# Kernel optimization log

Measured on AMD Instinct MI355X. Metric: run time of the kernel, lower is better.

Reference implementation:

```python
import jax, jax.numpy as jnp
import numpy as np

B, N, K, H = 2, 2048, 48, 128
SCALE = 30.0
LN_EPS = 1e-5


def _gather_nodes(nodes, idx):
    # nodes: [B,N,H], idx: [B,N,K] -> [B,N,K,H]
    return nodes[jnp.arange(nodes.shape[0])[:, None, None], idx]


def _ln(x, g, b):
    m = jnp.mean(x, axis=-1, keepdims=True)
    v = jnp.mean(jnp.square(x - m), axis=-1, keepdims=True)
    return (x - m) * jax.lax.rsqrt(v + LN_EPS) * g + b


def _gelu(x):
    return jax.nn.gelu(x, approximate=False)  # torch.nn.GELU default (erf)


def setup_inputs() -> dict:
    key = jax.random.key(0)
    ks = jax.random.split(key, 24)
    d = {}
    d["h_V"] = jax.random.normal(ks[0], (B, N, H), jnp.float32)
    d["h_E"] = jax.random.normal(ks[1], (B, N, K, H), jnp.float32)
    d["E_idx"] = jax.random.randint(ks[2], (B, N, K), 0, N)
    d["mask_V"] = (jax.random.uniform(ks[3], (B, N)) > 0.1).astype(jnp.float32)
    d["mask_attend"] = (jax.random.uniform(ks[4], (B, N, K)) > 0.1).astype(jnp.float32)
    s = 0.05
    # message MLP (node update): W1 in = 3H
    d["W1_w"] = s * jax.random.normal(ks[5], (3 * H, H), jnp.float32)
    d["W1_b"] = jnp.zeros((H,), jnp.float32)
    d["W2_w"] = s * jax.random.normal(ks[6], (H, H), jnp.float32)
    d["W2_b"] = jnp.zeros((H,), jnp.float32)
    d["W3_w"] = s * jax.random.normal(ks[7], (H, H), jnp.float32)
    d["W3_b"] = jnp.zeros((H,), jnp.float32)
    # message MLP (edge update)
    d["W11_w"] = s * jax.random.normal(ks[8], (3 * H, H), jnp.float32)
    d["W11_b"] = jnp.zeros((H,), jnp.float32)
    d["W12_w"] = s * jax.random.normal(ks[9], (H, H), jnp.float32)
    d["W12_b"] = jnp.zeros((H,), jnp.float32)
    d["W13_w"] = s * jax.random.normal(ks[10], (H, H), jnp.float32)
    d["W13_b"] = jnp.zeros((H,), jnp.float32)
    # FFN
    d["Win_w"] = s * jax.random.normal(ks[11], (H, 4 * H), jnp.float32)
    d["Win_b"] = jnp.zeros((4 * H,), jnp.float32)
    d["Wout_w"] = s * jax.random.normal(ks[12], (4 * H, H), jnp.float32)
    d["Wout_b"] = jnp.zeros((H,), jnp.float32)
    # layernorms
    for i, nm in enumerate(["ln1", "ln2", "ln3"]):
        d[nm + "_g"] = jnp.ones((H,), jnp.float32)
        d[nm + "_b"] = jnp.zeros((H,), jnp.float32)
    return d


def reference(h_V, h_E, E_idx, mask_V, mask_attend,
              W1_w, W1_b, W2_w, W2_b, W3_w, W3_b,
              W11_w, W11_b, W12_w, W12_b, W13_w, W13_b,
              Win_w, Win_b, Wout_w, Wout_b,
              ln1_g, ln1_b, ln2_g, ln2_b, ln3_g, ln3_b):
    # --- node message pass ---
    h_EV = jnp.concatenate([
        jnp.broadcast_to(h_V[:, :, None, :], h_E.shape),
        h_E,
        _gather_nodes(h_V, E_idx),
    ], axis=-1)  # [B,N,K,3H]
    h_msg = _gelu(h_EV @ W1_w + W1_b)
    h_msg = _gelu(h_msg @ W2_w + W2_b)
    h_msg = h_msg @ W3_w + W3_b
    h_msg = mask_attend[..., None] * h_msg
    dh = jnp.sum(h_msg, axis=-2) / SCALE  # [B,N,H]
    h_Vn = _ln(h_V + dh, ln1_g, ln1_b)
    # --- FFN ---
    dh = _gelu(h_Vn @ Win_w + Win_b) @ Wout_w + Wout_b
    h_Vn = _ln(h_Vn + dh, ln2_g, ln2_b)
    h_Vn = mask_V[..., None] * h_Vn
    # --- edge update ---
    h_EV2 = jnp.concatenate([
        jnp.broadcast_to(h_Vn[:, :, None, :], h_E.shape),
        h_E,
        _gather_nodes(h_Vn, E_idx),
    ], axis=-1)
    h_msg2 = _gelu(h_EV2 @ W11_w + W11_b)
    h_msg2 = _gelu(h_msg2 @ W12_w + W12_b)
    h_msg2 = h_msg2 @ W13_w + W13_b
    h_En = _ln(h_E + h_msg2, ln3_g, ln3_b)
    return (h_Vn, h_En)
```

## Files before the change

kernel.cpp:

```cpp
#include <hip/hip_runtime.h>
#include <hip/hip_bf16.h>

#define DEVINL __device__ __forceinline__

typedef __attribute__((ext_vector_type(8))) short short8;
typedef __attribute__((ext_vector_type(4))) float f32x4;

DEVINL unsigned short f2bf(float x) {
  __hip_bfloat16 h = __float2bfloat16(x);
  return __builtin_bit_cast(unsigned short, h);
}
DEVINL unsigned int pk2(float lo, float hi) {
  return (unsigned int)f2bf(lo) | ((unsigned int)f2bf(hi) << 16);
}
DEVINL float bf2f(unsigned short h) {
  union { unsigned int u; float f; } c; c.u = ((unsigned int)h) << 16;
  return c.f;
}
DEVINL float gelu_f(float x) {
  const float u = x * x;
  const float y = x * (0.7978845608f + 0.0356774081f * u);
  const float e = __expf(-2.0f * y);
  return x * __builtin_amdgcn_rcpf(1.0f + e);
}
DEVINL f32x4 mfma16(short8 a, short8 b, f32x4 c) {
  return __builtin_amdgcn_mfma_f32_16x16x32_bf16(a, b, c, 0, 0, 0);
}

template<int KSTEPS, int MT, int NT>
DEVINL void gemm_tiles(const unsigned short* Xl, int ldx,
                       const unsigned short* __restrict__ Wp,
                       int lane, int w, f32x4 (&acc)[MT][2])
{
  const int rr = lane & 15;
  const int kg = (lane >> 4) << 3;
  __builtin_amdgcn_s_setprio(1);
  #pragma unroll
  for (int t = 0; t < KSTEPS; ++t) {
    short8 a[MT];
    #pragma unroll
    for (int m = 0; m < MT; ++m)
      a[m] = *(const short8*)(Xl + (m * 16 + rr) * ldx + t * 32 + kg);
    #pragma unroll
    for (int c = 0; c < 2; ++c) {
      short8 bf = *(const short8*)(Wp + ((size_t)(t * NT + (w * 2 + c)) * 64 + lane) * 8);
      #pragma unroll
      for (int m = 0; m < MT; ++m)
        acc[m][c] = mfma16(a[m], bf, acc[m][c]);
    }
  }
  __builtin_amdgcn_s_setprio(0);
}

__global__ __launch_bounds__(256) void k_pack(
    const float* __restrict__ W1w,  const float* __restrict__ W2w,
    const float* __restrict__ W3w,  const float* __restrict__ W11w,
    const float* __restrict__ W12w, const float* __restrict__ W13w,
    const float* __restrict__ Winw, const float* __restrict__ Woutw,
    unsigned short* __restrict__ dst)
{
  const int f = blockIdx.x * 256 + threadIdx.x;
  if (f >= 36864) return;
  const float* src; int row0 = 0, Ncols = 128, NT = 8, lf;
  if (f < 20480) {
    const int seg = f >> 11; lf = f & 2047;
    switch (seg) {
      case 0: src = W1w;  row0 = 0;   break;
      case 1: src = W1w;  row0 = 128; break;
      case 2: src = W1w;  row0 = 256; break;
      case 3: src = W2w;  break;
      case 4: src = W3w;  break;
      case 5: src = W11w; row0 = 0;   break;
      case 6: src = W11w; row0 = 128; break;
      case 7: src = W11w; row0 = 256; break;
      case 8: src = W12w; break;
      default: src = W13w; break;
    }
  } else if (f < 28672) { src = Winw; lf = f - 20480; NT = 32; Ncols = 512; }
  else { src = Woutw; lf = f - 28672; }
  const int l = lf & 63;
  const int g = lf >> 6;
  const int c = g % NT;
  const int t = g / NT;
  const int r0 = row0 + t * 32 + ((l >> 4) << 3);
  const int col = c * 16 + (l & 15);
  short8 vv;
  #pragma unroll
  for (int b = 0; b < 8; ++b)
    vv[b] = (short)f2bf(src[(size_t)(r0 + b) * Ncols + col]);
  *(short8*)(dst + (size_t)f * 8) = vv;
}

__global__ __launch_bounds__(256) void k_pre(
    const float* __restrict__ X,
    const unsigned short* __restrict__ Wtp,
    const unsigned short* __restrict__ Wbp,
    const float* __restrict__ bias,
    float* __restrict__ P1, unsigned short* __restrict__ P3)
{
  __shared__ __align__(16) unsigned short Xs2[16 * 136];
  const int tid = threadIdx.x;
  const int lane = tid & 63;
  const int w = tid >> 6;
  const int rr = lane & 15;
  const int kg = (lane >> 4) << 3;
  const int row0 = blockIdx.x * 16;

  for (int e = tid; e < 512; e += 256) {
    const int r = e >> 5, q = (e & 31) << 2;
    float4 v = *(const float4*)(X + (size_t)(row0 + r) * 128 + q);
    uint2 pk; pk.x = pk2(v.x, v.y); pk.y = pk2(v.z, v.w);
    *(uint2*)(&Xs2[r * 136 + q]) = pk;
  }
  __syncthreads();

  const f32x4 zf = {0.f, 0.f, 0.f, 0.f};
  f32x4 a0[2] = {zf, zf}, a1[2] = {zf, zf};
  #pragma unroll
  for (int t = 0; t < 4; ++t) {
    const short8 a = *(const short8*)(&Xs2[rr * 136 + t * 32 + kg]);
    #pragma unroll
    for (int c = 0; c < 2; ++c) {
      short8 bt = *(const short8*)(Wtp + ((size_t)(t * 8 + (w * 2 + c)) * 64 + lane) * 8);
      a0[c] = mfma16(a, bt, a0[c]);
      short8 bb = *(const short8*)(Wbp + ((size_t)(t * 8 + (w * 2 + c)) * 64 + lane) * 8);
      a1[c] = mfma16(a, bb, a1[c]);
    }
  }
  #pragma unroll
  for (int c = 0; c < 2; ++c) {
    const int col = w * 32 + c * 16 + rr;
    const float b = bias[col];
    #pragma unroll
    for (int r = 0; r < 4; ++r) {
      const int row = row0 + ((lane >> 4) << 2) + r;
      P1[(size_t)row * 128 + col] = a0[c][r] + b;
      P3[(size_t)row * 128 + col] = f2bf(a1[c][r]);
    }
  }
}

template<bool HEB>
__global__ __launch_bounds__(256) void k_node_t(
    const float* __restrict__ hV, const float* __restrict__ hE,
    unsigned short* __restrict__ hEbOut,
    const int* __restrict__ Eidx, const float* __restrict__ maskA,
    const float* __restrict__ P1g, const unsigned short* __restrict__ P3g,
    const unsigned short* __restrict__ Wmidp,
    const unsigned short* __restrict__ W2p, const float* __restrict__ W2b,
    const unsigned short* __restrict__ W3p, const float* __restrict__ W3b,
    const float* __restrict__ ln1g, const float* __restrict__ ln1b,
    float* __restrict__ hVn1)
{
  __shared__ __align__(16) unsigned short Xs[48 * 136];
  __shared__ __align__(16) unsigned short Ms[48 * 136];
  __shared__ float maskv[48];
  __shared__ float dhs[128];
  __shared__ float red[2];

  const int tid = threadIdx.x;
  const int lane = tid & 63;
  const int w = tid >> 6;
  const int rr = lane & 15;
  const int g4 = (lane >> 4) << 2;
  const int bidx = (blockIdx.x & 7) * 512 + (blockIdx.x >> 3);
  const int bbase = bidx & ~2047;

  const float* hErow = hE + (size_t)bidx * 6144;
  const int* idxr = Eidx + (size_t)bidx * 48;

  if (tid < 48) maskv[tid] = maskA[(size_t)bidx * 48 + tid];

  for (int e = tid; e < 1536; e += 256) {
    const int r = e >> 5, q = (e & 31) << 2;
    float4 v = *(const float4*)(hErow + r * 128 + q);
    uint2 pk; pk.x = pk2(v.x, v.y); pk.y = pk2(v.z, v.w);
    *(uint2*)(&Xs[r * 136 + q]) = pk;
    if constexpr (HEB)
      *(uint2*)(hEbOut + (size_t)bidx * 6144 + r * 128 + q) = pk;
  }
  for (int e = tid; e < 768; e += 256) {
    const int r = e >> 4, q = (e & 15) << 3;
    const int j = idxr[r];
    *(short8*)(&Ms[r * 136 + q]) = *(const short8*)(P3g + (size_t)(bbase + j) * 128 + q);
  }
  const float p1c0 = P1g[(size_t)bidx * 128 + w * 32 + rr];
  const float p1c1 = P1g[(size_t)bidx * 128 + w * 32 + 16 + rr];
  __syncthreads();

  f32x4 acc[3][2];
  #pragma unroll
  for (int m = 0; m < 3; ++m)
    #pragma unroll
    for (int c = 0; c < 2; ++c)
      #pragma unroll
      for (int r = 0; r < 4; ++r) {
        const int row = m * 16 + g4 + r;
        const int col = w * 32 + c * 16 + rr;
        acc[m][c][r] = (c ? p1c1 : p1c0) + bf2f(Ms[row * 136 + col]);
      }

  gemm_tiles<4, 3, 8>(Xs, 136, Wmidp, lane, w, acc);
  #pragma unroll
  for (int m = 0; m < 3; ++m)
    #pragma unroll
    for (int c = 0; c < 2; ++c)
      #pragma unroll
      for (int r = 0; r < 4; ++r) {
        const int row = m * 16 + g4 + r;
        Ms[row * 136 + w * 32 + c * 16 + rr] = f2bf(gelu_f(acc[m][c][r]));
      }
  __syncthreads();

  const f32x4 zf = {0.f, 0.f, 0.f, 0.f};
  #pragma unroll
  for (int m = 0; m < 3; ++m) { acc[m][0] = zf; acc[m][1] = zf; }
  gemm_tiles<4, 3, 8>(Ms, 136, W2p, lane, w, acc);
  {
    const float b0 = W2b[w * 32 + rr], b1 = W2b[w * 32 + 16 + rr];
    #pragma unroll
    for (int m = 0; m < 3; ++m)
      #pragma unroll
      for (int c = 0; c < 2; ++c)
        #pragma unroll
        for (int r = 0; r < 4; ++r) {
          const int row = m * 16 + g4 + r;
          Xs[row * 136 + w * 32 + c * 16 + rr] = f2bf(gelu_f(acc[m][c][r] + (c ? b1 : b0)));
        }
  }
  __syncthreads();

  #pragma unroll
  for (int m = 0; m < 3; ++m) { acc[m][0] = zf; acc[m][1] = zf; }
  gemm_tiles<4, 3, 8>(Xs, 136, W3p, lane, w, acc);

  {
    const float b0 = W3b[w * 32 + rr], b1 = W3b[w * 32 + 16 + rr];
    float p0 = 0.f, p1 = 0.f;
    #pragma unroll
    for (int m = 0; m < 3; ++m)
      #pragma unroll
      for (int r = 0; r < 4; ++r) {
        const float mk = maskv[m * 16 + g4 + r];
        p0 += mk * (acc[m][0][r] + b0);
        p1 += mk * (acc[m][1][r] + b1);
      }
    p0 += __shfl_xor(p0, 16); p0 += __shfl_xor(p0, 32);
    p1 += __shfl_xor(p1, 16); p1 += __shfl_xor(p1, 32);
    if (lane < 16) { dhs[w * 32 + lane] = p0; dhs[w * 32 + 16 + lane] = p1; }
  }
  __syncthreads();

  if (tid < 64) {
    const float x0 = hV[(size_t)bidx * 128 + tid]      + dhs[tid]      * (1.0f / 30.0f);
    const float x1 = hV[(size_t)bidx * 128 + 64 + tid] + dhs[tid + 64] * (1.0f / 30.0f);
    float s = x0 + x1, q2 = x0 * x0 + x1 * x1;
    #pragma unroll
    for (int msk = 1; msk < 64; msk <<= 1) {
      s += __shfl_xor(s, msk);
      q2 += __shfl_xor(q2, msk);
    }
    if (tid == 0) {
      const float mean = s * (1.f / 128.f);
      red[0] = mean;
      red[1] = rsqrtf(q2 * (1.f / 128.f) - mean * mean + 1e-5f);
    }
  }
  __syncthreads();
  if (tid < 128) {
    const float x = hV[(size_t)bidx * 128 + tid] + dhs[tid] * (1.0f / 30.0f);
    hVn1[(size_t)bidx * 128 + tid] = (x - red[0]) * red[1] * ln1g[tid] + ln1b[tid];
  }
}

__global__ __launch_bounds__(256) void k_ffn(
    const float* __restrict__ hVn1,
    const unsigned short* __restrict__ Winp, const float* __restrict__ Winb,
    const unsigned short* __restrict__ Woutp, const float* __restrict__ Woutb,
    const float* __restrict__ ln2g, const float* __restrict__ ln2b,
    const float* __restrict__ maskV,
    const unsigned short* __restrict__ W11tp, const unsigned short* __restrict__ W11bp,
    const float* __restrict__ W11b,
    float* __restrict__ outV, float* __restrict__ P1, unsigned short* __restrict__ P3)
{
  __shared__ __align__(16) unsigned short Xs2[16 * 136];
  __shared__ __align__(16) unsigned short Ys[16 * 520];
  __shared__ __align__(16) unsigned short Ts[16 * 136];
  __shared__ float Rs[16 * 128];

  const int tid = threadIdx.x;
  const int lane = tid & 63;
  const int w = tid >> 6;
  const int rr = lane & 15;
  const int kg = (lane >> 4) << 3;
  const int row0 = blockIdx.x * 16;

  for (int e = tid; e < 512; e += 256) {
    const int r = e >> 5, q = (e & 31) << 2;
    float4 v = *(const float4*)(hVn1 + (size_t)(row0 + r) * 128 + q);
    uint2 pk; pk.x = pk2(v.x, v.y); pk.y = pk2(v.z, v.w);
    *(uint2*)(&Xs2[r * 136 + q]) = pk;
  }
  __syncthreads();

  const f32x4 zf = {0.f, 0.f, 0.f, 0.f};
  f32x4 acc1[8];
  #pragma unroll
  for (int c = 0; c < 8; ++c) acc1[c] = zf;
  #pragma unroll
  for (int t = 0; t < 4; ++t) {
    const short8 a = *(const short8*)(&Xs2[rr * 136 + t * 32 + kg]);
    #pragma unroll
    for (int c = 0; c < 8; ++c) {
      const short8 bf = *(const short8*)(Winp + ((size_t)(t * 32 + w * 8 + c) * 64 + lane) * 8);
      acc1[c] = mfma16(a, bf, acc1[c]);
    }
  }
  #pragma unroll
  for (int c = 0; c < 8; ++c) {
    const int col = w * 128 + c * 16 + rr;
    const float bias = Winb[col];
    #pragma unroll
    for (int r = 0; r < 4; ++r) {
      const int row = ((lane >> 4) << 2) + r;
      Ys[row * 520 + col] = f2bf(gelu_f(acc1[c][r] + bias));
    }
  }
  __syncthreads();

  f32x4 acc2[2];
  acc2[0] = zf; acc2[1] = zf;
  #pragma unroll 4
  for (int t = 0; t < 16; ++t) {
    const short8 a = *(const short8*)(&Ys[rr * 520 + t * 32 + kg]);
    #pragma unroll
    for (int c = 0; c < 2; ++c) {
      const short8 bf = *(const short8*)(Woutp + ((size_t)(t * 8 + w * 2 + c) * 64 + lane) * 8);
      acc2[c] = mfma16(a, bf, acc2[c]);
    }
  }
  #pragma unroll
  for (int c = 0; c < 2; ++c) {
    const int col = w * 32 + c * 16 + rr;
    const float bias = Woutb[col];
    #pragma unroll
    for (int r = 0; r < 4; ++r) {
      const int row = ((lane >> 4) << 2) + r;
      Rs[row * 128 + col] = acc2[c][r] + bias + hVn1[(size_t)(row0 + row) * 128 + col];
    }
  }
  __syncthreads();

  const float g0 = ln2g[lane], g1 = ln2g[lane + 64];
  const float be0 = ln2b[lane], be1 = ln2b[lane + 64];
  for (int i = 0; i < 4; ++i) {
    const int row = w * 4 + i;
    const int grow = row0 + row;
    const float x0 = Rs[row * 128 + lane], x1 = Rs[row * 128 + 64 + lane];
    float s = x0 + x1, q2 = x0 * x0 + x1 * x1;
    #pragma unroll
    for (int msk = 1; msk < 64; msk <<= 1) {
      s += __shfl_xor(s, msk);
      q2 += __shfl_xor(q2, msk);
    }
    const float mean = s * (1.f / 128.f);
    const float rstd = rsqrtf(q2 * (1.f / 128.f) - mean * mean + 1e-5f);
    const float mv = maskV[grow];
    const float y0 = ((x0 - mean) * rstd * g0 + be0) * mv;
    const float y1 = ((x1 - mean) * rstd * g1 + be1) * mv;
    outV[(size_t)grow * 128 + lane]      = y0;
    outV[(size_t)grow * 128 + 64 + lane] = y1;
    Ts[row * 136 + lane]      = f2bf(y0);
    Ts[row * 136 + 64 + lane] = f2bf(y1);
  }
  __syncthreads();

  f32x4 a0[2] = {zf, zf}, a1[2] = {zf, zf};
  #pragma unroll
  for (int t = 0; t < 4; ++t) {
    const short8 a = *(const short8*)(&Ts[rr * 136 + t * 32 + kg]);
    #pragma unroll
    for (int c = 0; c < 2; ++c) {
      short8 bt = *(const short8*)(W11tp + ((size_t)(t * 8 + (w * 2 + c)) * 64 + lane) * 8);
      a0[c] = mfma16(a, bt, a0[c]);
      short8 bb = *(const short8*)(W11bp + ((size_t)(t * 8 + (w * 2 + c)) * 64 + lane) * 8);
      a1[c] = mfma16(a, bb, a1[c]);
    }
  }
  #pragma unroll
  for (int c = 0; c < 2; ++c) {
    const int col = w * 32 + c * 16 + rr;
    const float b = W11b[col];
    #pragma unroll
    for (int r = 0; r < 4; ++r) {
      const int row = row0 + ((lane >> 4) << 2) + r;
      P1[(size_t)row * 128 + col] = a0[c][r] + b;
      P3[(size_t)row * 128 + col] = f2bf(a1[c][r]);
    }
  }
}

template<bool HEB>
__global__ __launch_bounds__(256) void k_edge_t(
    const float* __restrict__ hE, const unsigned short* __restrict__ hEb,
    const int* __restrict__ Eidx,
    const float* __restrict__ P1g, const unsigned short* __restrict__ P3g,
    const unsigned short* __restrict__ Wmidp,
    const unsigned short* __restrict__ W12p, const float* __restrict__ W12b,
    const unsigned short* __restrict__ W13p, const float* __restrict__ W13b,
    const float* __restrict__ ln3g, const float* __restrict__ ln3b,
    float* __restrict__ outE)
{
  __shared__ __align__(16) unsigned short Xs[48 * 136];
  __shared__ __align__(16) unsigned short Ms[48 * 136];
  __shared__ float sums[48 * 4];
  __shared__ float sqs[48 * 4];
  __shared__ float mr[96];

  const int tid = threadIdx.x;
  const int lane = tid & 63;
  const int w = tid >> 6;
  const int rr = lane & 15;
  const int g4 = (lane >> 4) << 2;
  const int bidx = (blockIdx.x & 7) * 512 + (blockIdx.x >> 3);
  const int bbase = bidx & ~2047;

  const int* idxr = Eidx + (size_t)bidx * 48;

  if constexpr (HEB) {
    for (int e = tid; e < 768; e += 256) {
      const int r = e >> 4, q = (e & 15) << 3;
      *(short8*)(&Xs[r * 136 + q]) = *(const short8*)(hEb + (size_t)bidx * 6144 + r * 128 + q);
    }
  } else {
    const float* hErow = hE + (size_t)bidx * 6144;
    for (int e = tid; e < 1536; e += 256) {
      const int r = e >> 5, q = (e & 31) << 2;
      float4 v = *(const float4*)(hErow + r * 128 + q);
      uint2 pk; pk.x = pk2(v.x, v.y); pk.y = pk2(v.z, v.w);
      *(uint2*)(&Xs[r * 136 + q]) = pk;
    }
  }
  for (int e = tid; e < 768; e += 256) {
    const int r = e >> 4, q = (e & 15) << 3;
    const int j = idxr[r];
    *(short8*)(&Ms[r * 136 + q]) = *(const short8*)(P3g + (size_t)(bbase + j) * 128 + q);
  }
  const float p1c0 = P1g[(size_t)bidx * 128 + w * 32 + rr];
  const float p1c1 = P1g[(size_t)bidx * 128 + w * 32 + 16 + rr];
  __syncthreads();

  f32x4 acc[3][2];
  float res[3][2][4];
  #pragma unroll
  for (int m = 0; m < 3; ++m)
    #pragma unroll
    for (int c = 0; c < 2; ++c)
      #pragma unroll
      for (int r = 0; r < 4; ++r) {
        const int row = m * 16 + g4 + r;
        const int col = w * 32 + c * 16 + rr;
        acc[m][c][r] = (c ? p1c1 : p1c0) + bf2f(Ms[row * 136 + col]);
        res[m][c][r] = bf2f(Xs[row * 136 + col]);
      }

  gemm_tiles<4, 3, 8>(Xs, 136, Wmidp, lane, w, acc);
  #pragma unroll
  for (int m = 0; m < 3; ++m)
    #pragma unroll
    for (int c = 0; c < 2; ++c)
      #pragma unroll
      for (int r = 0; r < 4; ++r) {
        const int row = m * 16 + g4 + r;
        Ms[row * 136 + w * 32 + c * 16 + rr] = f2bf(gelu_f(acc[m][c][r]));
      }
  __syncthreads();

  const f32x4 zf = {0.f, 0.f, 0.f, 0.f};
  #pragma unroll
  for (int m = 0; m < 3; ++m) { acc[m][0] = zf; acc[m][1] = zf; }
  gemm_tiles<4, 3, 8>(Ms, 136, W12p, lane, w, acc);
  {
    const float b0 = W12b[w * 32 + rr], b1 = W12b[w * 32 + 16 + rr];
    #pragma unroll
    for (int m = 0; m < 3; ++m)
      #pragma unroll
      for (int c = 0; c < 2; ++c)
        #pragma unroll
        for (int r = 0; r < 4; ++r) {
          const int row = m * 16 + g4 + r;
          Xs[row * 136 + w * 32 + c * 16 + rr] = f2bf(gelu_f(acc[m][c][r] + (c ? b1 : b0)));
        }
  }
  __syncthreads();

  #pragma unroll
  for (int m = 0; m < 3; ++m) { acc[m][0] = zf; acc[m][1] = zf; }
  gemm_tiles<4, 3, 8>(Xs, 136, W13p, lane, w, acc);

  {
    const float b0 = W13b[w * 32 + rr], b1 = W13b[w * 32 + 16 + rr];
    #pragma unroll
    for (int m = 0; m < 3; ++m)
      #pragma unroll
      for (int r = 0; r < 4; ++r) {
        const int row = m * 16 + g4 + r;
        acc[m][0][r] += b0 + res[m][0][r];
        acc[m][1][r] += b1 + res[m][1][r];
        float s = acc[m][0][r] + acc[m][1][r];
        float q2 = acc[m][0][r] * acc[m][0][r] + acc[m][1][r] * acc[m][1][r];
        s += __shfl_xor(s, 1); q2 += __shfl_xor(q2, 1);
        s += __shfl_xor(s, 2); q2 += __shfl_xor(q2, 2);
        s += __shfl_xor(s, 4); q2 += __shfl_xor(q2, 4);
        s += __shfl_xor(s, 8); q2 += __shfl_xor(q2, 8);
        if ((lane & 15) == 0) { sums[row * 4 + w] = s; sqs[row * 4 + w] = q2; }
      }
  }
  __syncthreads();
  if (tid < 48) {
    const float s = sums[tid * 4] + sums[tid * 4 + 1] + sums[tid * 4 + 2] + sums[tid * 4 + 3];
    const float q2 = sqs[tid * 4] + sqs[tid * 4 + 1] + sqs[tid * 4 + 2] + sqs[tid * 4 + 3];
    const float mean = s * (1.f / 128.f);
    mr[tid * 2] = mean;
    mr[tid * 2 + 1] = rsqrtf(q2 * (1.f / 128.f) - mean * mean + 1e-5f);
  }
  __syncthreads();
  {
    const float g0 = ln3g[w * 32 + rr], g1 = ln3g[w * 32 + 16 + rr];
    const float be0 = ln3b[w * 32 + rr], be1 = ln3b[w * 32 + 16 + rr];
    #pragma unroll
    for (int m = 0; m < 3; ++m)
      #pragma unroll
      for (int r = 0; r < 4; ++r) {
        const int row = m * 16 + g4 + r;
        const float mean = mr[row * 2], rstd = mr[row * 2 + 1];
        const size_t base = (size_t)bidx * 6144 + (size_t)row * 128 + w * 32 + rr;
        outE[base]      = (acc[m][0][r] - mean) * rstd * g0 + be0;
        outE[base + 16] = (acc[m][1][r] - mean) * rstd * g1 + be1;
      }
  }
}

extern "C" void kernel_launch(void* const* d_in, const int* in_sizes, int n_in,
                              void* d_out, int out_size, void* d_ws, size_t ws_size,
                              hipStream_t stream) {
  const float* hV    = (const float*)d_in[0];
  const float* hE    = (const float*)d_in[1];
  const int*   Eidx  = (const int*)d_in[2];
  const float* maskV = (const float*)d_in[3];
  const float* maskA = (const float*)d_in[4];
  const float* W1w  = (const float*)d_in[5];  const float* W1b  = (const float*)d_in[6];
  const float* W2w  = (const float*)d_in[7];  const float* W2b  = (const float*)d_in[8];
  const float* W3w  = (const float*)d_in[9];  const float* W3b  = (const float*)d_in[10];
  const float* W11w = (const float*)d_in[11]; const float* W11b = (const float*)d_in[12];
  const float* W12w = (const float*)d_in[13]; const float* W12b = (const float*)d_in[14];
  const float* W13w = (const float*)d_in[15]; const float* W13b = (const float*)d_in[16];
  const float* Winw = (const float*)d_in[17]; const float* Winb = (const float*)d_in[18];
  const float* Woutw= (const float*)d_in[19]; const float* Woutb= (const float*)d_in[20];
  const float* ln1g = (const float*)d_in[21]; const float* ln1b = (const float*)d_in[22];
  const float* ln2g = (const float*)d_in[23]; const float* ln2b = (const float*)d_in[24];
  const float* ln3g = (const float*)d_in[25]; const float* ln3b = (const float*)d_in[26];

  float* outV = (float*)d_out;
  float* outE = outV + (size_t)4096 * 128;

  char* ws = (char*)d_ws;
  float* hVn1 = (float*)ws;
  float* P1   = (float*)(ws + (size_t)2 * 1024 * 1024);
  unsigned short* P3 = (unsigned short*)(ws + (size_t)4 * 1024 * 1024);
  unsigned short* Wp = (unsigned short*)(ws + (size_t)5 * 1024 * 1024);
  unsigned short* hEb = (unsigned short*)(ws + (size_t)6 * 1024 * 1024);

  const size_t NEED = (size_t)6 * 1024 * 1024 + (size_t)4096 * 48 * 128 * 2;
  const bool heb = ws_size >= NEED;

  const unsigned short* W1top_p  = Wp;
  const unsigned short* W1mid_p  = Wp + (size_t)2048 * 8;
  const unsigned short* W1bot_p  = Wp + (size_t)4096 * 8;
  const unsigned short* W2p      = Wp + (size_t)6144 * 8;
  const unsigned short* W3p      = Wp + (size_t)8192 * 8;
  const unsigned short* W11top_p = Wp + (size_t)10240 * 8;
  const unsigned short* W11mid_p = Wp + (size_t)12288 * 8;
  const unsigned short* W11bot_p = Wp + (size_t)14336 * 8;
  const unsigned short* W12p     = Wp + (size_t)16384 * 8;
  const unsigned short* W13p     = Wp + (size_t)18432 * 8;
  const unsigned short* Winp     = Wp + (size_t)20480 * 8;
  const unsigned short* Woutp    = Wp + (size_t)28672 * 8;

  k_pack<<<144, 256, 0, stream>>>(W1w, W2w, W3w, W11w, W12w, W13w, Winw, Woutw, Wp);
  k_pre<<<256, 256, 0, stream>>>(hV, W1top_p, W1bot_p, W1b, P1, P3);

  if (heb)
    k_node_t<true><<<4096, 256, 0, stream>>>(hV, hE, hEb, Eidx, maskA, P1, P3,
                                             W1mid_p, W2p, W2b, W3p, W3b,
                                             ln1g, ln1b, hVn1);
  else
    k_node_t<false><<<4096, 256, 0, stream>>>(hV, hE, hEb, Eidx, maskA, P1, P3,
                                              W1mid_p, W2p, W2b, W3p, W3b,
                                              ln1g, ln1b, hVn1);

  k_ffn<<<256, 256, 0, stream>>>(hVn1, Winp, Winb, Woutp, Woutb,
                                 ln2g, ln2b, maskV,
                                 W11top_p, W11bot_p, W11b,
                                 outV, P1, P3);

  if (heb)
    k_edge_t<true><<<4096, 256, 0, stream>>>(hE, hEb, Eidx, P1, P3,
                                             W11mid_p, W12p, W12b, W13p, W13b,
                                             ln3g, ln3b, outE);
  else
    k_edge_t<false><<<4096, 256, 0, stream>>>(hE, hEb, Eidx, P1, P3,
                                              W11mid_p, W12p, W12b, W13p, W13b,
                                              ln3g, ln3b, outE);
}
```

Measured before the change: 142.9 us.

## Stream h_E directly into MFMA fragments and drop the Xs LDS buffer

```diff
diff --git a/kernel.cpp b/kernel.cpp
--- a/kernel.cpp
+++ b/kernel.cpp
@@ -140,10 +140,10 @@
   }
 }
 
-template<bool HEB>
-__global__ __launch_bounds__(256) void k_node_t(
+template<bool HEBW>
+__global__ __launch_bounds__(256, 6) void k_node_t(
     const float* __restrict__ hV, const float* __restrict__ hE,
-    unsigned short* __restrict__ hEbOut,
+    unsigned short* __restrict__ hEb,
     const int* __restrict__ Eidx, const float* __restrict__ maskA,
     const float* __restrict__ P1g, const unsigned short* __restrict__ P3g,
     const unsigned short* __restrict__ Wmidp,
@@ -152,43 +152,62 @@
     const float* __restrict__ ln1g, const float* __restrict__ ln1b,
     float* __restrict__ hVn1)
 {
-  __shared__ __align__(16) unsigned short Xs[48 * 136];
   __shared__ __align__(16) unsigned short Ms[48 * 136];
   __shared__ float maskv[48];
   __shared__ float dhs[128];
-  __shared__ float red[2];
 
   const int tid = threadIdx.x;
   const int lane = tid & 63;
   const int w = tid >> 6;
   const int rr = lane & 15;
   const int g4 = (lane >> 4) << 2;
+  const int kg = (lane >> 4) << 3;
   const int bidx = (blockIdx.x & 7) * 512 + (blockIdx.x >> 3);
   const int bbase = bidx & ~2047;
-
-  const float* hErow = hE + (size_t)bidx * 6144;
   const int* idxr = Eidx + (size_t)bidx * 48;
 
   if (tid < 48) maskv[tid] = maskA[(size_t)bidx * 48 + tid];
-
-  for (int e = tid; e < 1536; e += 256) {
-    const int r = e >> 5, q = (e & 31) << 2;
-    float4 v = *(const float4*)(hErow + r * 128 + q);
-    uint2 pk; pk.x = pk2(v.x, v.y); pk.y = pk2(v.z, v.w);
-    *(uint2*)(&Xs[r * 136 + q]) = pk;
-    if constexpr (HEB)
-      *(uint2*)(hEbOut + (size_t)bidx * 6144 + r * 128 + q) = pk;
-  }
-  for (int e = tid; e < 768; e += 256) {
+  #pragma unroll
+  for (int i = 0; i < 3; ++i) {
+    const int e = i * 256 + tid;
     const int r = e >> 4, q = (e & 15) << 3;
     const int j = idxr[r];
     *(short8*)(&Ms[r * 136 + q]) = *(const short8*)(P3g + (size_t)(bbase + j) * 128 + q);
   }
   const float p1c0 = P1g[(size_t)bidx * 128 + w * 32 + rr];
   const float p1c1 = P1g[(size_t)bidx * 128 + w * 32 + 16 + rr];
-  __syncthreads();
-
+
+  const f32x4 zf = {0.f, 0.f, 0.f, 0.f};
   f32x4 acc[3][2];
+  #pragma unroll
+  for (int m = 0; m < 3; ++m) { acc[m][0] = zf; acc[m][1] = zf; }
+  {
+    const float* Arow = hE + (size_t)bidx * 6144;
+    unsigned short* Hrow = hEb + (size_t)bidx * 6144;
+    __builtin_amdgcn_s_setprio(1);
+    #pragma unroll
+    for (int t = 0; t < 4; ++t) {
+      const short8 bf0 = *(const short8*)(Wmidp + ((size_t)(t * 8 + w * 2) * 64 + lane) * 8);
+      const short8 bf1 = *(const short8*)(Wmidp + ((size_t)(t * 8 + w * 2 + 1) * 64 + lane) * 8);
+      #pragma unroll
+      for (int m = 0; m < 3; ++m) {
+        const float* p = Arow + (m * 16 + rr) * 128 + t * 32 + kg;
+        float4 v0 = *(const float4*)p;
+        float4 v1 = *(const float4*)(p + 4);
+        uint4 pk;
+        pk.x = pk2(v0.x, v0.y); pk.y = pk2(v0.z, v0.w);
+        pk.z = pk2(v1.x, v1.y); pk.w = pk2(v1.z, v1.w);
+        if (HEBW && w == 0)
+          *(uint4*)(Hrow + (m * 16 + rr) * 128 + t * 32 + kg) = pk;
+        const short8 a = __builtin_bit_cast(short8, pk);
+        acc[m][0] = mfma16(a, bf0, acc[m][0]);
+        acc[m][1] = mfma16(a, bf1, acc[m][1]);
+      }
+    }
+    __builtin_amdgcn_s_setprio(0);
+  }
+  __syncthreads();
+
   #pragma unroll
   for (int m = 0; m < 3; ++m)
     #pragma unroll
@@ -197,10 +216,21 @@
       for (int r = 0; r < 4; ++r) {
         const int row = m * 16 + g4 + r;
         const int col = w * 32 + c * 16 + rr;
-        acc[m][c][r] = (c ? p1c1 : p1c0) + bf2f(Ms[row * 136 + col]);
-      }
-
-  gemm_tiles<4, 3, 8>(Xs, 136, Wmidp, lane, w, acc);
+        const float v = acc[m][c][r] + (c ? p1c1 : p1c0) + bf2f(Ms[row * 136 + col]);
+        Ms[row * 136 + col] = f2bf(gelu_f(v));
+      }
+  __syncthreads();
+
+  {
+    const float b0 = W2b[w * 32 + rr], b1 = W2b[w * 32 + 16 + rr];
+    #pragma unroll
+    for (int m = 0; m < 3; ++m) {
+      acc[m][0] = (f32x4){b0, b0, b0, b0};
+      acc[m][1] = (f32x4){b1, b1, b1, b1};
+    }
+  }
+  gemm_tiles<4, 3, 8>(Ms, 136, W2p, lane, w, acc);
+  __syncthreads();
   #pragma unroll
   for (int m = 0; m < 3; ++m)
     #pragma unroll
@@ -212,38 +242,25 @@
       }
   __syncthreads();
 
-  const f32x4 zf = {0.f, 0.f, 0.f, 0.f};
-  #pragma unroll
-  for (int m = 0; m < 3; ++m) { acc[m][0] = zf; acc[m][1] = zf; }
-  gemm_tiles<4, 3, 8>(Ms, 136, W2p, lane, w, acc);
-  {
-    const float b0 = W2b[w * 32 + rr], b1 = W2b[w * 32 + 16 + rr];
-    #pragma unroll
-    for (int m = 0; m < 3; ++m)
-      #pragma unroll
-      for (int c = 0; c < 2; ++c)
-        #pragma unroll
-        for (int r = 0; r < 4; ++r) {
-          const int row = m * 16 + g4 + r;
-          Xs[row * 136 + w * 32 + c * 16 + rr] = f2bf(gelu_f(acc[m][c][r] + (c ? b1 : b0)));
-        }
-  }
-  __syncthreads();
-
-  #pragma unroll
-  for (int m = 0; m < 3; ++m) { acc[m][0] = zf; acc[m][1] = zf; }
-  gemm_tiles<4, 3, 8>(Xs, 136, W3p, lane, w, acc);
-
   {
     const float b0 = W3b[w * 32 + rr], b1 = W3b[w * 32 + 16 + rr];
+    #pragma unroll
+    for (int m = 0; m < 3; ++m) {
+      acc[m][0] = (f32x4){b0, b0, b0, b0};
+      acc[m][1] = (f32x4){b1, b1, b1, b1};
+    }
+  }
+  gemm_tiles<4, 3, 8>(Ms, 136, W3p, lane, w, acc);
+
+  {
     float p0 = 0.f, p1 = 0.f;
     #pragma unroll
     for (int m = 0; m < 3; ++m)
       #pragma unroll
       for (int r = 0; r < 4; ++r) {
         const float mk = maskv[m * 16 + g4 + r];
-        p0 += mk * (acc[m][0][r] + b0);
-        p1 += mk * (acc[m][1][r] + b1);
+        p0 += mk * acc[m][0][r];
+        p1 += mk * acc[m][1][r];
       }
     p0 += __shfl_xor(p0, 16); p0 += __shfl_xor(p0, 32);
     p1 += __shfl_xor(p1, 16); p1 += __shfl_xor(p1, 32);
@@ -251,25 +268,22 @@
   }
   __syncthreads();
 
-  if (tid < 64) {
-    const float x0 = hV[(size_t)bidx * 128 + tid]      + dhs[tid]      * (1.0f / 30.0f);
-    const float x1 = hV[(size_t)bidx * 128 + 64 + tid] + dhs[tid + 64] * (1.0f / 30.0f);
-    float s = x0 + x1, q2 = x0 * x0 + x1 * x1;
+  {
+    const float x0 = hV[(size_t)bidx * 128 + lane]      + dhs[lane]      * (1.0f / 30.0f);
+    const float x1 = hV[(size_t)bidx * 128 + 64 + lane] + dhs[lane + 64] * (1.0f / 30.0f);
+    float s = x0 + x1, sq = x0 * x0 + x1 * x1;
     #pragma unroll
     for (int msk = 1; msk < 64; msk <<= 1) {
       s += __shfl_xor(s, msk);
-      q2 += __shfl_xor(q2, msk);
-    }
-    if (tid == 0) {
-      const float mean = s * (1.f / 128.f);
-      red[0] = mean;
-      red[1] = rsqrtf(q2 * (1.f / 128.f) - mean * mean + 1e-5f);
-    }
-  }
-  __syncthreads();
-  if (tid < 128) {
-    const float x = hV[(size_t)bidx * 128 + tid] + dhs[tid] * (1.0f / 30.0f);
-    hVn1[(size_t)bidx * 128 + tid] = (x - red[0]) * red[1] * ln1g[tid] + ln1b[tid];
+      sq += __shfl_xor(sq, msk);
+    }
+    const float mean = s * (1.f / 128.f);
+    const float rstd = rsqrtf(sq * (1.f / 128.f) - mean * mean + 1e-5f);
+    if (lane < 32) {
+      const int col = w * 32 + lane;
+      const float xx = hV[(size_t)bidx * 128 + col] + dhs[col] * (1.0f / 30.0f);
+      hVn1[(size_t)bidx * 128 + col] = (xx - mean) * rstd * ln1g[col] + ln1b[col];
+    }
   }
 }
 
@@ -401,7 +415,7 @@
 }
 
 template<bool HEB>
-__global__ __launch_bounds__(256) void k_edge_t(
+__global__ __launch_bounds__(256, 6) void k_edge_t(
     const float* __restrict__ hE, const unsigned short* __restrict__ hEb,
     const int* __restrict__ Eidx,
     const float* __restrict__ P1g, const unsigned short* __restrict__ P3g,
@@ -411,7 +425,6 @@
     const float* __restrict__ ln3g, const float* __restrict__ ln3b,
     float* __restrict__ outE)
 {
-  __shared__ __align__(16) unsigned short Xs[48 * 136];
   __shared__ __align__(16) unsigned short Ms[48 * 136];
   __shared__ float sums[48 * 4];
   __shared__ float sqs[48 * 4];
@@ -422,36 +435,53 @@
   const int w = tid >> 6;
   const int rr = lane & 15;
   const int g4 = (lane >> 4) << 2;
+  const int kg = (lane >> 4) << 3;
   const int bidx = (blockIdx.x & 7) * 512 + (blockIdx.x >> 3);
   const int bbase = bidx & ~2047;
-
   const int* idxr = Eidx + (size_t)bidx * 48;
 
-  if constexpr (HEB) {
-    for (int e = tid; e < 768; e += 256) {
-      const int r = e >> 4, q = (e & 15) << 3;
-      *(short8*)(&Xs[r * 136 + q]) = *(const short8*)(hEb + (size_t)bidx * 6144 + r * 128 + q);
-    }
-  } else {
-    const float* hErow = hE + (size_t)bidx * 6144;
-    for (int e = tid; e < 1536; e += 256) {
-      const int r = e >> 5, q = (e & 31) << 2;
-      float4 v = *(const float4*)(hErow + r * 128 + q);
-      uint2 pk; pk.x = pk2(v.x, v.y); pk.y = pk2(v.z, v.w);
-      *(uint2*)(&Xs[r * 136 + q]) = pk;
-    }
-  }
-  for (int e = tid; e < 768; e += 256) {
+  #pragma unroll
+  for (int i = 0; i < 3; ++i) {
+    const int e = i * 256 + tid;
     const int r = e >> 4, q = (e & 15) << 3;
     const int j = idxr[r];
     *(short8*)(&Ms[r * 136 + q]) = *(const short8*)(P3g + (size_t)(bbase + j) * 128 + q);
   }
   const float p1c0 = P1g[(size_t)bidx * 128 + w * 32 + rr];
   const float p1c1 = P1g[(size_t)bidx * 128 + w * 32 + 16 + rr];
-  __syncthreads();
-
+
+  const f32x4 zf = {0.f, 0.f, 0.f, 0.f};
   f32x4 acc[3][2];
-  float res[3][2][4];
+  #pragma unroll
+  for (int m = 0; m < 3; ++m) { acc[m][0] = zf; acc[m][1] = zf; }
+  {
+    __builtin_amdgcn_s_setprio(1);
+    #pragma unroll
+    for (int t = 0; t < 4; ++t) {
+      const short8 bf0 = *(const short8*)(Wmidp + ((size_t)(t * 8 + w * 2) * 64 + lane) * 8);
+      const short8 bf1 = *(const short8*)(Wmidp + ((size_t)(t * 8 + w * 2 + 1) * 64 + lane) * 8);
+      #pragma unroll
+      for (int m = 0; m < 3; ++m) {
+        short8 a;
+        if constexpr (HEB) {
+          a = *(const short8*)(hEb + (size_t)bidx * 6144 + (m * 16 + rr) * 128 + t * 32 + kg);
+        } else {
+          const float* p = hE + (size_t)bidx * 6144 + (m * 16 + rr) * 128 + t * 32 + kg;
+          float4 v0 = *(const float4*)p;
+          float4 v1 = *(const float4*)(p + 4);
+          uint4 pk;
+          pk.x = pk2(v0.x, v0.y); pk.y = pk2(v0.z, v0.w);
+          pk.z = pk2(v1.x, v1.y); pk.w = pk2(v1.z, v1.w);
+          a = __builtin_bit_cast(short8, pk);
+        }
+        acc[m][0] = mfma16(a, bf0, acc[m][0]);
+        acc[m][1] = mfma16(a, bf1, acc[m][1]);
+      }
+    }
+    __builtin_amdgcn_s_setprio(0);
+  }
+  __syncthreads();
+
   #pragma unroll
   for (int m = 0; m < 3; ++m)
     #pragma unroll
@@ -460,11 +490,21 @@
       for (int r = 0; r < 4; ++r) {
         const int row = m * 16 + g4 + r;
         const int col = w * 32 + c * 16 + rr;
-        acc[m][c][r] = (c ? p1c1 : p1c0) + bf2f(Ms[row * 136 + col]);
-        res[m][c][r] = bf2f(Xs[row * 136 + col]);
-      }
-
-  gemm_tiles<4, 3, 8>(Xs, 136, Wmidp, lane, w, acc);
+        const float v = acc[m][c][r] + (c ? p1c1 : p1c0) + bf2f(Ms[row * 136 + col]);
+        Ms[row * 136 + col] = f2bf(gelu_f(v));
+      }
+  __syncthreads();
+
+  {
+    const float b0 = W12b[w * 32 + rr], b1 = W12b[w * 32 + 16 + rr];
+    #pragma unroll
+    for (int m = 0; m < 3; ++m) {
+      acc[m][0] = (f32x4){b0, b0, b0, b0};
+      acc[m][1] = (f32x4){b1, b1, b1, b1};
+    }
+  }
+  gemm_tiles<4, 3, 8>(Ms, 136, W12p, lane, w, acc);
+  __syncthreads();
   #pragma unroll
   for (int m = 0; m < 3; ++m)
     #pragma unroll
@@ -476,46 +516,39 @@
       }
   __syncthreads();
 
-  const f32x4 zf = {0.f, 0.f, 0.f, 0.f};
-  #pragma unroll
-  for (int m = 0; m < 3; ++m) { acc[m][0] = zf; acc[m][1] = zf; }
-  gemm_tiles<4, 3, 8>(Ms, 136, W12p, lane, w, acc);
-  {
-    const float b0 = W12b[w * 32 + rr], b1 = W12b[w * 32 + 16 + rr];
-    #pragma unroll
-    for (int m = 0; m < 3; ++m)
-      #pragma unroll
-      for (int c = 0; c < 2; ++c)
-        #pragma unroll
-        for (int r = 0; r < 4; ++r) {
-          const int row = m * 16 + g4 + r;
-          Xs[row * 136 + w * 32 + c * 16 + rr] = f2bf(gelu_f(acc[m][c][r] + (c ? b1 : b0)));
-        }
-  }
-  __syncthreads();
-
-  #pragma unroll
-  for (int m = 0; m < 3; ++m) { acc[m][0] = zf; acc[m][1] = zf; }
-  gemm_tiles<4, 3, 8>(Xs, 136, W13p, lane, w, acc);
-
   {
     const float b0 = W13b[w * 32 + rr], b1 = W13b[w * 32 + 16 + rr];
     #pragma unroll
-    for (int m = 0; m < 3; ++m)
-      #pragma unroll
-      for (int r = 0; r < 4; ++r) {
-        const int row = m * 16 + g4 + r;
-        acc[m][0][r] += b0 + res[m][0][r];
-        acc[m][1][r] += b1 + res[m][1][r];
-        float s = acc[m][0][r] + acc[m][1][r];
-        float q2 = acc[m][0][r] * acc[m][0][r] + acc[m][1][r] * acc[m][1][r];
-        s += __shfl_xor(s, 1); q2 += __shfl_xor(q2, 1);
-        s += __shfl_xor(s, 2); q2 += __shfl_xor(q2, 2);
-        s += __shfl_xor(s, 4); q2 += __shfl_xor(q2, 4);
-        s += __shfl_xor(s, 8); q2 += __shfl_xor(q2, 8);
-        if ((lane & 15) == 0) { sums[row * 4 + w] = s; sqs[row * 4 + w] = q2; }
-      }
-  }
+    for (int m = 0; m < 3; ++m) {
+      acc[m][0] = (f32x4){b0, b0, b0, b0};
+      acc[m][1] = (f32x4){b1, b1, b1, b1};
+    }
+  }
+  gemm_tiles<4, 3, 8>(Ms, 136, W13p, lane, w, acc);
+
+  #pragma unroll
+  for (int m = 0; m < 3; ++m)
+    #pragma unroll
+    for (int r = 0; r < 4; ++r) {
+      const int row = m * 16 + g4 + r;
+      float r0, r1;
+      if constexpr (HEB) {
+        r0 = bf2f(hEb[(size_t)bidx * 6144 + row * 128 + w * 32 + rr]);
+        r1 = bf2f(hEb[(size_t)bidx * 6144 + row * 128 + w * 32 + 16 + rr]);
+      } else {
+        r0 = hE[(size_t)bidx * 6144 + row * 128 + w * 32 + rr];
+        r1 = hE[(size_t)bidx * 6144 + row * 128 + w * 32 + 16 + rr];
+      }
+      acc[m][0][r] += r0;
+      acc[m][1][r] += r1;
+      float s = acc[m][0][r] + acc[m][1][r];
+      float q2 = acc[m][0][r] * acc[m][0][r] + acc[m][1][r] * acc[m][1][r];
+      s += __shfl_xor(s, 1); q2 += __shfl_xor(q2, 1);
+      s += __shfl_xor(s, 2); q2 += __shfl_xor(q2, 2);
+      s += __shfl_xor(s, 4); q2 += __shfl_xor(q2, 4);
+      s += __shfl_xor(s, 8); q2 += __shfl_xor(q2, 8);
+      if ((lane & 15) == 0) { sums[row * 4 + w] = s; sqs[row * 4 + w] = q2; }
+    }
   __syncthreads();
   if (tid < 48) {
     const float s = sums[tid * 4] + sums[tid * 4 + 1] + sums[tid * 4 + 2] + sums[tid * 4 + 3];
```

Result: slower. 166.7 us (+16.7%).

## Fold W3 projection after masked sum to replace per-edge GEMM with GEMV

Applied to the files above, without the earlier changes.

```diff
diff --git a/kernel.cpp b/kernel.cpp
--- a/kernel.cpp
+++ b/kernel.cpp
@@ -148,7 +148,7 @@
     const float* __restrict__ P1g, const unsigned short* __restrict__ P3g,
     const unsigned short* __restrict__ Wmidp,
     const unsigned short* __restrict__ W2p, const float* __restrict__ W2b,
-    const unsigned short* __restrict__ W3p, const float* __restrict__ W3b,
+    const float* __restrict__ W3w, const float* __restrict__ W3b,
     const float* __restrict__ ln1g, const float* __restrict__ ln1b,
     float* __restrict__ hVn1)
 {
@@ -156,7 +156,8 @@
   __shared__ __align__(16) unsigned short Ms[48 * 136];
   __shared__ float maskv[48];
   __shared__ float dhs[128];
-  __shared__ float red[2];
+  __shared__ float mv[256];
+  __shared__ float red[1];
 
   const int tid = threadIdx.x;
   const int lane = tid & 63;
@@ -188,6 +189,12 @@
   const float p1c1 = P1g[(size_t)bidx * 128 + w * 32 + 16 + rr];
   __syncthreads();
 
+  if (tid == 0) {
+    float nm = 0.f;
+    for (int i = 0; i < 48; ++i) nm += maskv[i];
+    red[0] = nm;
+  }
+
   f32x4 acc[3][2];
   #pragma unroll
   for (int m = 0; m < 3; ++m)
@@ -212,38 +219,24 @@
       }
   __syncthreads();
 
-  const f32x4 zf = {0.f, 0.f, 0.f, 0.f};
-  #pragma unroll
-  for (int m = 0; m < 3; ++m) { acc[m][0] = zf; acc[m][1] = zf; }
+  {
+    const float b0 = W2b[w * 32 + rr], b1 = W2b[w * 32 + 16 + rr];
+    #pragma unroll
+    for (int m = 0; m < 3; ++m) {
+      acc[m][0] = (f32x4){b0, b0, b0, b0};
+      acc[m][1] = (f32x4){b1, b1, b1, b1};
+    }
+  }
   gemm_tiles<4, 3, 8>(Ms, 136, W2p, lane, w, acc);
   {
-    const float b0 = W2b[w * 32 + rr], b1 = W2b[w * 32 + 16 + rr];
-    #pragma unroll
-    for (int m = 0; m < 3; ++m)
-      #pragma unroll
-      for (int c = 0; c < 2; ++c)
-        #pragma unroll
-        for (int r = 0; r < 4; ++r) {
-          const int row = m * 16 + g4 + r;
-          Xs[row * 136 + w * 32 + c * 16 + rr] = f2bf(gelu_f(acc[m][c][r] + (c ? b1 : b0)));
-        }
-  }
-  __syncthreads();
-
-  #pragma unroll
-  for (int m = 0; m < 3; ++m) { acc[m][0] = zf; acc[m][1] = zf; }
-  gemm_tiles<4, 3, 8>(Xs, 136, W3p, lane, w, acc);
-
-  {
-    const float b0 = W3b[w * 32 + rr], b1 = W3b[w * 32 + 16 + rr];
     float p0 = 0.f, p1 = 0.f;
     #pragma unroll
     for (int m = 0; m < 3; ++m)
       #pragma unroll
       for (int r = 0; r < 4; ++r) {
         const float mk = maskv[m * 16 + g4 + r];
-        p0 += mk * (acc[m][0][r] + b0);
-        p1 += mk * (acc[m][1][r] + b1);
+        p0 += mk * gelu_f(acc[m][0][r]);
+        p1 += mk * gelu_f(acc[m][1][r]);
       }
     p0 += __shfl_xor(p0, 16); p0 += __shfl_xor(p0, 32);
     p1 += __shfl_xor(p1, 16); p1 += __shfl_xor(p1, 32);
@@ -251,25 +244,33 @@
   }
   __syncthreads();
 
-  if (tid < 64) {
-    const float x0 = hV[(size_t)bidx * 128 + tid]      + dhs[tid]      * (1.0f / 30.0f);
-    const float x1 = hV[(size_t)bidx * 128 + 64 + tid] + dhs[tid + 64] * (1.0f / 30.0f);
-    float s = x0 + x1, q2 = x0 * x0 + x1 * x1;
+  {
+    const int col = tid & 127;
+    const int k0 = (tid >> 7) * 64;
+    float part = 0.f;
+    #pragma unroll 8
+    for (int k = 0; k < 64; ++k)
+      part = fmaf(dhs[k0 + k], W3w[(size_t)(k0 + k) * 128 + col], part);
+    mv[tid] = part;
+  }
+  __syncthreads();
+
+  if (w == 0) {
+    const float nm = red[0];
+    const float dh0 = mv[lane]      + mv[128 + lane]      + nm * W3b[lane];
+    const float dh1 = mv[64 + lane] + mv[192 + lane]      + nm * W3b[64 + lane];
+    const float x0 = hV[(size_t)bidx * 128 + lane]      + dh0 * (1.0f / 30.0f);
+    const float x1 = hV[(size_t)bidx * 128 + 64 + lane] + dh1 * (1.0f / 30.0f);
+    float s = x0 + x1, sq = x0 * x0 + x1 * x1;
     #pragma unroll
     for (int msk = 1; msk < 64; msk <<= 1) {
       s += __shfl_xor(s, msk);
-      q2 += __shfl_xor(q2, msk);
-    }
-    if (tid == 0) {
-      const float mean = s * (1.f / 128.f);
-      red[0] = mean;
-      red[1] = rsqrtf(q2 * (1.f / 128.f) - mean * mean + 1e-5f);
-    }
-  }
-  __syncthreads();
-  if (tid < 128) {
-    const float x = hV[(size_t)bidx * 128 + tid] + dhs[tid] * (1.0f / 30.0f);
-    hVn1[(size_t)bidx * 128 + tid] = (x - red[0]) * red[1] * ln1g[tid] + ln1b[tid];
+      sq += __shfl_xor(sq, msk);
+    }
+    const float mean = s * (1.f / 128.f);
+    const float rstd = rsqrtf(sq * (1.f / 128.f) - mean * mean + 1e-5f);
+    hVn1[(size_t)bidx * 128 + lane]      = (x0 - mean) * rstd * ln1g[lane] + ln1b[lane];
+    hVn1[(size_t)bidx * 128 + 64 + lane] = (x1 - mean) * rstd * ln1g[64 + lane] + ln1b[64 + lane];
   }
 }
 
@@ -578,7 +579,6 @@
   const unsigned short* W1mid_p  = Wp + (size_t)2048 * 8;
   const unsigned short* W1bot_p  = Wp + (size_t)4096 * 8;
   const unsigned short* W2p      = Wp + (size_t)6144 * 8;
-  const unsigned short* W3p      = Wp + (size_t)8192 * 8;
   const unsigned short* W11top_p = Wp + (size_t)10240 * 8;
   const unsigned short* W11mid_p = Wp + (size_t)12288 * 8;
   const unsigned short* W11bot_p = Wp + (size_t)14336 * 8;
@@ -592,11 +592,11 @@
 
   if (heb)
     k_node_t<true><<<4096, 256, 0, stream>>>(hV, hE, hEb, Eidx, maskA, P1, P3,
-                                             W1mid_p, W2p, W2b, W3p, W3b,
+                                             W1mid_p, W2p, W2b, W3w, W3b,
                                              ln1g, ln1b, hVn1);
   else
     k_node_t<false><<<4096, 256, 0, stream>>>(hV, hE, hEb, Eidx, maskA, P1, P3,
-                                              W1mid_p, W2p, W2b, W3p, W3b,
+                                              W1mid_p, W2p, W2b, W3w, W3b,
                                               ln1g, ln1b, hVn1);
 
   k_ffn<<<256, 256, 0, stream>>>(hVn1, Winp, Winb, Woutp, Woutb,
```

After: 137.9 us. 1.04x faster.
